# Kernel tuning notes

Measured on AMD Instinct MI355X. Metric: run time of the kernel, lower is better.

## Reference

```python
import jax, jax.numpy as jnp
import numpy as np

B, N, F_, D = 4, 1024, 10, 16
DOUT = 16
EMB = 10  # nn.LayerNorm(10)
NF = N * F_


def setup_inputs() -> dict:
    key = jax.random.key(0)
    ks = jax.random.split(key, 8)
    x = jax.random.normal(ks[0], (B, N, F_, D), dtype=jnp.float32)
    factor_embeddings = jax.random.normal(ks[1], (F_, EMB), dtype=jnp.float32)
    grid_embeddings = jax.random.normal(ks[2], (N, EMB), dtype=jnp.float32)
    supports = jax.random.uniform(ks[3], (NF, NF), dtype=jnp.float32)
    # parameters
    ln_gamma = jnp.ones((EMB,), jnp.float32)
    ln_beta = jnp.zeros((EMB,), jnp.float32)
    W_gcn = jax.random.normal(ks[4], (D, DOUT), dtype=jnp.float32) * 0.05
    b_gcn = jnp.zeros((DOUT,), jnp.float32)
    W_out = jax.random.normal(ks[5], (F_ * DOUT, DOUT), dtype=jnp.float32) * 0.05
    b_out = jnp.zeros((DOUT,), jnp.float32)
    return {"x": x, "factor_embeddings": factor_embeddings,
            "grid_embeddings": grid_embeddings, "supports": supports,
            "ln_gamma": ln_gamma, "ln_beta": ln_beta,
            "W_gcn": W_gcn, "b_gcn": b_gcn, "W_out": W_out, "b_out": b_out}


def _layernorm(h, g, b, eps=1e-12):
    mu = jnp.mean(h, axis=-1, keepdims=True)
    var = jnp.mean(jnp.square(h - mu), axis=-1, keepdims=True)
    return (h - mu) / jnp.sqrt(var + eps) * g + b


def reference(x, factor_embeddings, grid_embeddings, supports,
              ln_gamma, ln_beta, W_gcn, b_gcn, W_out, b_out):
    b_, n_, f_, d_ = x.shape
    nf = n_ * f_
    xf = x.reshape(b_, nf, d_)

    # --- factor-graph attention (DEAD CODE in the original forward: the
    # masked factor_graphs tensor is never used; dense_to_sparse reads
    # `supports` directly). Computed here for shape fidelity only. ---
    gfe = _layernorm(factor_embeddings[None, :, :] + grid_embeddings[:, None, :],
                     ln_gamma, ln_beta)               # (N, F, EMB)
    factor_graphs = jax.nn.softmax(jnp.einsum('nfd,ngd->nfg', gfe, gfe), axis=-1)
    _ = factor_graphs  # the (NF,NF) repeat * supports is unused -> omitted

    # --- GCNConv(normalize=True) on the dense-to-sparse(supports) graph ---
    # add_remaining_self_loops: keep existing diag weights, fill zeros with 1
    diag = jnp.diagonal(supports)
    idx = jnp.arange(nf)
    A = supports.at[idx, idx].set(jnp.where(diag == 0, 1.0, diag))
    deg = A.sum(axis=0)                               # scatter_add over col (target)
    dinv = jnp.where(deg > 0, jax.lax.rsqrt(deg), 0.0)
    A_norm = dinv[:, None] * A * dinv[None, :]        # norm_ij = d_i^-1/2 A_ij d_j^-1/2

    h = jnp.einsum('bid,do->bio', xf, W_gcn)          # GCN linear (no bias)
    h = jnp.einsum('ij,bio->bjo', A_norm, h) + b_gcn  # aggregate src i -> dst j
    h = jax.nn.relu(h)                                # (B, NF, DOUT)

    h = h.reshape(b_, n_, f_ * h.shape[-1])           # (B, N, F*DOUT)
    return h @ W_out + b_out                          # (B, N, DOUT)
```

## Files before the change

kernel.cpp:

```cpp
#include <hip/hip_runtime.h>
#include <cstdint>
#include <cstddef>

#define NF 10240

typedef _Float16 half8_t __attribute__((ext_vector_type(8)));
typedef float floatx4 __attribute__((ext_vector_type(4)));

__global__ __launch_bounds__(256) void k_deg(const float* __restrict__ sup,
                                             float* __restrict__ deg) {
  const int tid = threadIdx.x;
  const int c = blockIdx.x * 1024 + tid * 4;
  const int r0 = blockIdx.y * 128;
  const float* p = sup + (size_t)r0 * NF + c;
  float a[4] = {0.f, 0.f, 0.f, 0.f};
  for (int k = 0; k < 128; ++k) {
    const float4 v = *(const float4*)p;
    p += NF;
    a[0] += v.x; a[1] += v.y; a[2] += v.z; a[3] += v.w;
  }
#pragma unroll
  for (int e = 0; e < 4; ++e) {
    const int i = c + e;
    if (i >= r0 && i < r0 + 128) {
      if (sup[(size_t)i * NF + i] == 0.f) a[e] += 1.f;
    }
  }
#pragma unroll
  for (int e = 0; e < 4; ++e) atomicAdd(&deg[c + e], a[e]);
}

__global__ __launch_bounds__(256) void k_g(const float* __restrict__ x,
                                           const float* __restrict__ Wg,
                                           const float* __restrict__ deg,
                                           float* __restrict__ dinv,
                                           _Float16* __restrict__ gp) {
  __shared__ float w[256];
  w[threadIdx.x] = Wg[threadIdx.x];
  __syncthreads();
  const int t = blockIdx.x * 256 + threadIdx.x;
  const int b = t / NF;
  const int i = t % NF;
  float xv[16];
  const float* xp = x + (size_t)t * 16;
#pragma unroll
  for (int d = 0; d < 16; ++d) xv[d] = xp[d];
  const float dg = deg[i];
  const float di = dg > 0.f ? rsqrtf(dg) : 0.f;
  if (b == 0) dinv[i] = di;
  const int base = ((i >> 3) * 64 + b * 16) * 8 + (i & 7);
#pragma unroll
  for (int o = 0; o < 16; ++o) {
    float h = 0.f;
#pragma unroll
    for (int d = 0; d < 16; ++d) h += xv[d] * w[d * 16 + o];
    gp[base + o * 8] = (_Float16)(h * di);
  }
}

__global__ __launch_bounds__(256) void k_gemm(const float* __restrict__ sup,
                                              const half8_t* __restrict__ gp8,
                                              float* __restrict__ Cp,
                                              int kRange, int nchunk) {
  __shared__ float ldsA[64 * 65];
  const int tid = threadIdx.x;
  const int lane = tid & 63;
  const int w = tid >> 6;
  const int x = lane & 15;
  const int q = lane >> 4;
  const int jbase = blockIdx.x * 64;
  const int kbase0 = blockIdx.y * kRange;

  floatx4 acc[4] = {};

  const int stage_r = tid >> 4;
  const int stage_c = (tid & 15) * 4;

  for (int ch = 0; ch < nchunk; ++ch) {
    const int kbase = kbase0 + ch * 64;
    __syncthreads();
#pragma unroll
    for (int pass = 0; pass < 4; ++pass) {
      const int r = stage_r + pass * 16;
      const int gi = kbase + r;
      float4 v = *(const float4*)(sup + (size_t)gi * NF + jbase + stage_c);
      const int gj = jbase + stage_c;
      if (gi == gj     && v.x == 0.f) v.x = 1.f;
      if (gi == gj + 1 && v.y == 0.f) v.y = 1.f;
      if (gi == gj + 2 && v.z == 0.f) v.z = 1.f;
      if (gi == gj + 3 && v.w == 0.f) v.w = 1.f;
      float* d = &ldsA[stage_c * 65 + r];
      d[0] = v.x; d[65] = v.y; d[130] = v.z; d[195] = v.w;
    }
    __syncthreads();
    const int k8base = kbase >> 3;
#pragma unroll
    for (int s = 0; s < 2; ++s) {
      const half8_t bfrag = gp8[(k8base + s * 4 + q) * 64 + w * 16 + x];
#pragma unroll
      for (int ms = 0; ms < 4; ++ms) {
        const float* ap = &ldsA[(ms * 16 + x) * 65 + s * 32 + q * 8];
        half8_t afrag;
#pragma unroll
        for (int jj = 0; jj < 8; ++jj) afrag[jj] = (_Float16)ap[jj];
        acc[ms] = __builtin_amdgcn_mfma_f32_16x16x32_f16(afrag, bfrag,
                                                         acc[ms], 0, 0, 0);
      }
    }
  }

  const size_t pbase = (size_t)blockIdx.y * NF;
#pragma unroll
  for (int ms = 0; ms < 4; ++ms) {
#pragma unroll
    for (int r = 0; r < 4; ++r) {
      const int j = jbase + ms * 16 + q * 4 + r;
      Cp[(pbase + j) * 64 + w * 16 + x] = acc[ms][r];
    }
  }
}

__global__ __launch_bounds__(256) void k_out(const float* __restrict__ Cp,
                                             const float* __restrict__ dinv,
                                             const float* __restrict__ bgcn,
                                             const float* __restrict__ Wout,
                                             const float* __restrict__ bout,
                                             float* __restrict__ out, int S) {
  __shared__ float wl[2560];
  __shared__ float tmp[640];
  const int n = blockIdx.x;
  const int t = threadIdx.x;
  for (int idx = t; idx < 2560; idx += 256) wl[idx] = Wout[idx];
  if (t < 160) {
    const int f = t >> 4, o = t & 15;
    const int j = n * 10 + f;
    const float di = dinv[j];
    const float bg = bgcn[o];
    for (int b = 0; b < 4; ++b) {
      float s = 0.f;
      for (int p = 0; p < S; ++p)
        s += Cp[((size_t)(p * NF + j)) * 64 + b * 16 + o];
      const float v = di * s + bg;
      tmp[b * 160 + t] = v > 0.f ? v : 0.f;
    }
  }
  __syncthreads();
  if (t < 64) {
    const int b = t >> 4, oc = t & 15;
    float acc = bout[oc];
    for (int k = 0; k < 160; ++k) acc += tmp[b * 160 + k] * wl[k * 16 + oc];
    out[((size_t)(b * 1024 + n)) * 16 + oc] = acc;
  }
}

extern "C" void kernel_launch(void* const* d_in, const int* in_sizes, int n_in,
                              void* d_out, int out_size, void* d_ws,
                              size_t ws_size, hipStream_t stream) {
  const float* x   = (const float*)d_in[0];
  const float* sup = (const float*)d_in[3];
  const float* Wg  = (const float*)d_in[6];
  const float* bg  = (const float*)d_in[7];
  const float* Wo  = (const float*)d_in[8];
  const float* bo  = (const float*)d_in[9];
  float* out = (float*)d_out;

  char* ws = (char*)d_ws;
  float*     deg  = (float*)ws;
  float*     dinv = (float*)(ws + 40960);
  _Float16*  gp   = (_Float16*)(ws + 81920);
  float*     Cp   = (float*)(ws + 81920 + 1310720);

  const size_t head = 81920 + 1310720;
  const int S = (ws_size >= head + (size_t)8 * NF * 64 * 4) ? 8 : 4;
  const int kRange = NF / S;
  const int nchunk = kRange / 64;

  hipMemsetAsync(deg, 0, NF * sizeof(float), stream);
  k_deg<<<dim3(10, 80), 256, 0, stream>>>(sup, deg);
  k_g<<<160, 256, 0, stream>>>(x, Wg, deg, dinv, gp);
  k_gemm<<<dim3(160, S), 256, 0, stream>>>(sup, (const half8_t*)gp, Cp,
                                           kRange, nchunk);
  k_out<<<1024, 256, 0, stream>>>(Cp, dinv, bg, Wo, bo, out, S);
}
```

Before: 666.3 us.

## Fuse degree pass with fp16 conversion of adjacency and feed GEMM half-precision input

After: 676.7 us. No clear change (+1.6%).

```diff
diff --git a/kernel.cpp b/kernel.cpp
--- a/kernel.cpp
+++ b/kernel.cpp
@@ -5,29 +5,48 @@
 #define NF 10240
 
 typedef _Float16 half8_t __attribute__((ext_vector_type(8)));
+typedef _Float16 half4_t __attribute__((ext_vector_type(4)));
 typedef float floatx4 __attribute__((ext_vector_type(4)));
 
-__global__ __launch_bounds__(256) void k_deg(const float* __restrict__ sup,
-                                             float* __restrict__ deg) {
-  const int tid = threadIdx.x;
-  const int c = blockIdx.x * 1024 + tid * 4;
-  const int r0 = blockIdx.y * 128;
-  const float* p = sup + (size_t)r0 * NF + c;
-  float a[4] = {0.f, 0.f, 0.f, 0.f};
-  for (int k = 0; k < 128; ++k) {
-    const float4 v = *(const float4*)p;
-    p += NF;
-    a[0] += v.x; a[1] += v.y; a[2] += v.z; a[3] += v.w;
+__global__ __launch_bounds__(256) void k_prep(const float* __restrict__ sup,
+                                              _Float16* __restrict__ Ah,
+                                              float* __restrict__ deg) {
+  __shared__ float lsum[8 * 128];
+  const int t = threadIdx.x;
+  const int j0 = blockIdx.x * 128;
+  const int i0 = blockIdx.y * 320;
+  const int cq = t & 31;
+  const int rg = t >> 5;
+  const int j = j0 + cq * 4;
+  float4 s4 = {0.f, 0.f, 0.f, 0.f};
+  const bool diagBlock = (i0 < j0 + 128) && (j0 < i0 + 320);
+#pragma unroll 4
+  for (int p = 0; p < 40; ++p) {
+    const int i = i0 + p * 8 + rg;
+    float4 v = *(const float4*)(sup + (size_t)i * NF + j);
+    if (diagBlock) {
+      if (i == j     && v.x == 0.f) v.x = 1.f;
+      if (i == j + 1 && v.y == 0.f) v.y = 1.f;
+      if (i == j + 2 && v.z == 0.f) v.z = 1.f;
+      if (i == j + 3 && v.w == 0.f) v.w = 1.f;
+    }
+    s4.x += v.x; s4.y += v.y; s4.z += v.z; s4.w += v.w;
+    half4_t h;
+    h[0] = (_Float16)v.x; h[1] = (_Float16)v.y;
+    h[2] = (_Float16)v.z; h[3] = (_Float16)v.w;
+    *(half4_t*)(Ah + (size_t)i * NF + j) = h;
   }
+  lsum[rg * 128 + cq * 4 + 0] = s4.x;
+  lsum[rg * 128 + cq * 4 + 1] = s4.y;
+  lsum[rg * 128 + cq * 4 + 2] = s4.z;
+  lsum[rg * 128 + cq * 4 + 3] = s4.w;
+  __syncthreads();
+  if (t < 128) {
+    float s = 0.f;
 #pragma unroll
-  for (int e = 0; e < 4; ++e) {
-    const int i = c + e;
-    if (i >= r0 && i < r0 + 128) {
-      if (sup[(size_t)i * NF + i] == 0.f) a[e] += 1.f;
-    }
+    for (int r = 0; r < 8; ++r) s += lsum[r * 128 + t];
+    atomicAdd(&deg[j0 + t], s);
   }
-#pragma unroll
-  for (int e = 0; e < 4; ++e) atomicAdd(&deg[c + e], a[e]);
 }
 
 __global__ __launch_bounds__(256) void k_g(const float* __restrict__ x,
@@ -58,11 +77,11 @@
   }
 }
 
-__global__ __launch_bounds__(256) void k_gemm(const float* __restrict__ sup,
-                                              const half8_t* __restrict__ gp8,
-                                              float* __restrict__ Cp,
-                                              int kRange, int nchunk) {
-  __shared__ float ldsA[64 * 65];
+__global__ __launch_bounds__(256) void k_gemm2(const _Float16* __restrict__ Ah,
+                                               const half8_t* __restrict__ gp8,
+                                               float* __restrict__ Cp,
+                                               int kRange, int nchunk) {
+  __shared__ unsigned int lds32[64 * 36];
   const int tid = threadIdx.x;
   const int lane = tid & 63;
   const int w = tid >> 6;
@@ -70,27 +89,25 @@
   const int q = lane >> 4;
   const int jbase = blockIdx.x * 64;
   const int kbase0 = blockIdx.y * kRange;
+  const int cq = tid & 15;
+  const int ip = tid >> 4;
 
   floatx4 acc[4] = {};
-
-  const int stage_r = tid >> 4;
-  const int stage_c = (tid & 15) * 4;
 
   for (int ch = 0; ch < nchunk; ++ch) {
     const int kbase = kbase0 + ch * 64;
     __syncthreads();
 #pragma unroll
-    for (int pass = 0; pass < 4; ++pass) {
-      const int r = stage_r + pass * 16;
-      const int gi = kbase + r;
-      float4 v = *(const float4*)(sup + (size_t)gi * NF + jbase + stage_c);
-      const int gj = jbase + stage_c;
-      if (gi == gj     && v.x == 0.f) v.x = 1.f;
-      if (gi == gj + 1 && v.y == 0.f) v.y = 1.f;
-      if (gi == gj + 2 && v.z == 0.f) v.z = 1.f;
-      if (gi == gj + 3 && v.w == 0.f) v.w = 1.f;
-      float* d = &ldsA[stage_c * 65 + r];
-      d[0] = v.x; d[65] = v.y; d[130] = v.z; d[195] = v.w;
+    for (int p = 0; p < 2; ++p) {
+      const int il = p * 32 + ip * 2;
+      const _Float16* r0 = Ah + (size_t)(kbase + il) * NF + jbase + cq * 4;
+      const ushort4 a0 = *(const ushort4*)r0;
+      const ushort4 a1 = *(const ushort4*)(r0 + NF);
+      unsigned int* d = &lds32[(cq * 4) * 36 + p * 16 + ip];
+      d[0]   = (unsigned)a0.x | ((unsigned)a1.x << 16);
+      d[36]  = (unsigned)a0.y | ((unsigned)a1.y << 16);
+      d[72]  = (unsigned)a0.z | ((unsigned)a1.z << 16);
+      d[108] = (unsigned)a0.w | ((unsigned)a1.w << 16);
     }
     __syncthreads();
     const int k8base = kbase >> 3;
@@ -99,10 +116,8 @@
       const half8_t bfrag = gp8[(k8base + s * 4 + q) * 64 + w * 16 + x];
 #pragma unroll
       for (int ms = 0; ms < 4; ++ms) {
-        const float* ap = &ldsA[(ms * 16 + x) * 65 + s * 32 + q * 8];
-        half8_t afrag;
-#pragma unroll
-        for (int jj = 0; jj < 8; ++jj) afrag[jj] = (_Float16)ap[jj];
+        const half8_t afrag = *(const half8_t*)((const _Float16*)lds32 +
+                                (ms * 16 + x) * 72 + s * 32 + q * 8);
         acc[ms] = __builtin_amdgcn_mfma_f32_16x16x32_f16(afrag, bfrag,
                                                          acc[ms], 0, 0, 0);
       }
@@ -168,17 +183,17 @@
   float*     deg  = (float*)ws;
   float*     dinv = (float*)(ws + 40960);
   _Float16*  gp   = (_Float16*)(ws + 81920);
-  float*     Cp   = (float*)(ws + 81920 + 1310720);
+  _Float16*  Ah   = (_Float16*)(ws + 1392640);
+  float*     Cp   = (float*)(ws + 1392640 + 209715200);
 
-  const size_t head = 81920 + 1310720;
-  const int S = (ws_size >= head + (size_t)8 * NF * 64 * 4) ? 8 : 4;
+  const int S = 8;
   const int kRange = NF / S;
   const int nchunk = kRange / 64;
 
   hipMemsetAsync(deg, 0, NF * sizeof(float), stream);
-  k_deg<<<dim3(10, 80), 256, 0, stream>>>(sup, deg);
+  k_prep<<<dim3(80, 32), 256, 0, stream>>>(sup, Ah, deg);
   k_g<<<160, 256, 0, stream>>>(x, Wg, deg, dinv, gp);
-  k_gemm<<<dim3(160, S), 256, 0, stream>>>(sup, (const half8_t*)gp, Cp,
-                                           kRange, nchunk);
+  k_gemm2<<<dim3(160, S), 256, 0, stream>>>(Ah, (const half8_t*)gp, Cp,
+                                            kRange, nchunk);
   k_out<<<1024, 256, 0, stream>>>(Cp, dinv, bg, Wo, bo, out, S);
 }
```
